# Performance work log

Hardware: AMD Instinct MI355X
Metric: run time of the kernel (lower is better)

## Reference

```python
import jax, jax.numpy as jnp
import numpy as np

B, T, D, U = 64, 512, 512, 512


def setup_inputs() -> dict:
    key = jax.random.key(0)
    ks = jax.random.split(key, 8)
    s_in = 1.0 / np.sqrt(D)
    s_rec = 1.0 / np.sqrt(U)
    return {
        "xf": jax.random.normal(ks[0], (B, T, D), jnp.float32),
        "xb": jax.random.normal(ks[1], (B, T, D), jnp.float32),
        "Wf": jax.random.normal(ks[2], (D, 4 * U), jnp.float32) * s_in,
        "Uf": jax.random.normal(ks[3], (U, 4 * U), jnp.float32) * s_rec,
        "bf": jnp.zeros((4 * U,), jnp.float32),
        "Wb": jax.random.normal(ks[4], (D, 4 * U), jnp.float32) * s_in,
        "Ub": jax.random.normal(ks[5], (U, 4 * U), jnp.float32) * s_rec,
        "bb": jnp.zeros((4 * U,), jnp.float32),
    }


def _lstm(x, W, Urec, b):
    # x: [B,T,D]; Keras gate order i,f,g,o. Inference mode: dropout inactive.
    u = Urec.shape[0]
    xz = jnp.einsum("btd,dk->btk", x, W) + b  # precompute input projection [B,T,4u]
    xz = jnp.swapaxes(xz, 0, 1)  # [T,B,4u] for scan

    def step(carry, z_t):
        h, c = carry
        z = z_t + h @ Urec  # [B,4u]
        i = jax.nn.sigmoid(z[:, :u])
        f = jax.nn.sigmoid(z[:, u:2 * u])
        g = jnp.tanh(z[:, 2 * u:3 * u])
        o = jax.nn.sigmoid(z[:, 3 * u:])
        c = f * c + i * g
        h = o * jnp.tanh(c)
        return (h, c), h

    nb = x.shape[0]
    h0 = jnp.zeros((nb, u), x.dtype)
    c0 = jnp.zeros((nb, u), x.dtype)
    _, hs = jax.lax.scan(step, (h0, c0), xz)  # hs: [T,B,u]
    return jnp.swapaxes(hs, 0, 1)  # [B,T,u]


def reference(xf, xb, Wf, Uf, bf, Wb, Ub, bb):
    fwd = _lstm(xf, Wf, Uf, bf)
    bwd = _lstm(xb, Wb, Ub, bb)
    return jnp.concatenate([fwd, bwd], axis=-1)  # [B,T,2U]
```

## Files before the change

kernel.cpp:

```cpp
#include <hip/hip_runtime.h>
#include <stdint.h>


typedef _Float16 f16;
typedef _Float16 f16x8 __attribute__((ext_vector_type(8)));
typedef float    f32x4 __attribute__((ext_vector_type(4)));
typedef unsigned long long u64;

typedef __attribute__((address_space(1))) const void* gas_ptr;
typedef __attribute__((address_space(3))) void* las_ptr;

__device__ inline void gl_lds16(const void* g, void* l) {
    __builtin_amdgcn_global_load_lds((gas_ptr)g, (las_ptr)l, 16, 0, 0);
}

#define SENT64 0x7F7F7F7F7F7F7F7FULL


__global__ void k_cvt(const float* __restrict__ src, f16* __restrict__ dst, int n8) {
    int i = blockIdx.x * 256 + threadIdx.x;
    if (i >= n8) return;
    const float4* s = (const float4*)src;
    float4 a = s[2 * i], b = s[2 * i + 1];
    f16x8 o = {(f16)a.x, (f16)a.y, (f16)a.z, (f16)a.w,
               (f16)b.x, (f16)b.y, (f16)b.z, (f16)b.w};
    *(f16x8*)(dst + 8 * (size_t)i) = o;
}

__global__ void k_tcvt(const float* __restrict__ src, f16* __restrict__ dst) {
    int tid = blockIdx.x * 256 + threadIdx.x;
    int kc = tid >> 11;
    int n  = tid & 2047;
    f16x8 o;
#pragma unroll
    for (int j = 0; j < 8; ++j)
        o[j] = (f16)src[(size_t)(kc * 8 + j) * 2048 + n];
    *(f16x8*)(dst + (size_t)n * 512 + kc * 8) = o;
}


__global__ void k_fill(f16* __restrict__ ring, int CT, int zero0) {
    size_t i = ((size_t)blockIdx.x * 256 + threadIdx.x) * 8;
    const size_t slot = 65536;
    size_t total = (size_t)(CT + 1) * slot;
    if (i >= total) return;
    u64 fillv = SENT64;
    if (i < slot) { if (!zero0) return; fillv = 0; }
    union { u64 u[2]; f16x8 v; } t; t.u[0] = fillv; t.u[1] = fillv;
    *(f16x8*)(ring + i) = t.v;
}

__global__ void k_copyslot(f16* __restrict__ ring, int CT) {
    size_t i = (size_t)(blockIdx.x * 256 + threadIdx.x) * 8;
    f16x8 v = *(const f16x8*)(ring + (size_t)CT * 65536 + i);
    *(f16x8*)(ring + i) = v;
}


__global__ __launch_bounds__(256) void k_proj(
    const f16* __restrict__ x16, const f16* __restrict__ WT,
    const float* __restrict__ bfw, const float* __restrict__ bbw,
    f16* __restrict__ xz, int t0, int CT, int lct) {
    __shared__ f16 smem[16384];
    f16* As = smem;
    f16* Bs = smem + 8192;

    const int tid = threadIdx.x;
    const int l = tid & 63, v = tid >> 6;
    const int mt = blockIdx.x, nt = blockIdx.y, d = blockIdx.z;
    const int wm = v >> 1, wn = v & 1;
    const int lr4 = l >> 4, c16 = l & 15;

    f32x4 acc[4][4];
#pragma unroll
    for (int i = 0; i < 4; ++i)
#pragma unroll
        for (int j = 0; j < 4; ++j) acc[i][j] = (f32x4)0.f;

    auto stage = [&](int kk, int buf) {
#pragma unroll
        for (int rd = 0; rd < 2; ++rd) {
            int idx = rd * 256 + tid;
            int r = idx >> 2, kp = idx & 3;
            int m = mt * 128 + r;
            int b = m >> lct, tc = m & (CT - 1);
            const f16* ga = x16 + (((size_t)(d * 64 + b) * 512 + (t0 + tc)) * 512 + kk * 32 + kp * 8);
            gl_lds16(ga, &As[buf * 4096 + (rd * 256 + v * 64) * 8]);
        }
#pragma unroll
        for (int rd = 0; rd < 2; ++rd) {
            int idx = rd * 256 + tid;
            int r = idx >> 2, kp = idx & 3;
            const f16* gb = WT + ((size_t)(d * 2048 + nt * 128 + r) * 512 + kk * 32 + kp * 8);
            gl_lds16(gb, &Bs[buf * 4096 + (rd * 256 + v * 64) * 8]);
        }
    };

    stage(0, 0);
    for (int kk = 0; kk < 16; ++kk) {
        __syncthreads();
        if (kk < 15) stage(kk + 1, (kk + 1) & 1);
        int buf = kk & 1;
        f16x8 af[4], bfr[4];
#pragma unroll
        for (int mf = 0; mf < 4; ++mf)
            af[mf] = *(const f16x8*)&As[buf * 4096 + (wm * 64 + mf * 16 + c16) * 32 + lr4 * 8];
#pragma unroll
        for (int nf = 0; nf < 4; ++nf)
            bfr[nf] = *(const f16x8*)&Bs[buf * 4096 + (wn * 64 + nf * 16 + c16) * 32 + lr4 * 8];
#pragma unroll
        for (int mf = 0; mf < 4; ++mf)
#pragma unroll
            for (int nf = 0; nf < 4; ++nf)
                acc[mf][nf] = __builtin_amdgcn_mfma_f32_16x16x32_f16(af[mf], bfr[nf], acc[mf][nf], 0, 0, 0);
    }
    __syncthreads();

    const float* bias = d ? bbw : bfw;
    float bv[4];
#pragma unroll
    for (int nf = 0; nf < 4; ++nf) bv[nf] = bias[nt * 128 + wn * 64 + nf * 16 + c16];

    f16* Cs = smem;
#pragma unroll
    for (int mf = 0; mf < 4; ++mf)
#pragma unroll
        for (int nf = 0; nf < 4; ++nf)
#pragma unroll
            for (int r = 0; r < 4; ++r) {
                int row = wm * 64 + mf * 16 + lr4 * 4 + r;
                int col = wn * 64 + nf * 16 + c16;
                Cs[row * 128 + col] = (f16)(acc[mf][nf][r] + bv[nf]);
            }
    __syncthreads();
#pragma unroll
    for (int ch = 0; ch < 8; ++ch) {
        int flat = ch * 256 + tid;
        int row = flat >> 4, cc = flat & 15;
        int m = mt * 128 + row;
        int b = m >> lct, tc = m & (CT - 1);
        f16x8 val = *(const f16x8*)&Cs[row * 128 + cc * 8];
        *(f16x8*)&xz[((size_t)(d * 64 + b) * CT + tc) * 2048 + nt * 128 + cc * 8] = val;
    }
}


__global__ __launch_bounds__(256, 1) void k_recur(
    const f16* __restrict__ xz, const f16* __restrict__ UT,
    f16* __restrict__ ring, float* __restrict__ cbuf,
    float* __restrict__ out, int t0, int CT) {
    __shared__ f16 xzsm[2][2048];
    __shared__ f16 wsm[4][128];
    __shared__ f16 hsm[8192];

    const int tid = threadIdx.x;
    const int l = tid & 63, v = tid >> 6;
    const int bx = blockIdx.x;
    const int d   = bx >> 6;
    const int grp = (bx >> 4) & 3;
    const int wg  = bx & 15;
    const int wu0 = wg * 32;
    const int lr4 = l >> 4;
    const int du  = (l & 15) >> 2;
    const int gid = l & 3;
    const int gidx = d * 4 + grp;

    int unitloc[2], nstd[2];
#pragma unroll
    for (int nf = 0; nf < 2; ++nf) {
        int u = wu0 + v * 8 + nf * 4 + du;
        unitloc[nf] = v * 8 + nf * 4 + du;
        nstd[nf] = gid * 512 + u;
    }

    f16x8 Ufr[2][16];
#pragma unroll
    for (int nf = 0; nf < 2; ++nf)
#pragma unroll
        for (int kk = 0; kk < 16; ++kk)
            Ufr[nf][kk] = *(const f16x8*)&UT[((size_t)d * 2048 + nstd[nf]) * 512 + kk * 32 + lr4 * 8];

    float cst[2][4];
#pragma unroll
    for (int nf = 0; nf < 2; ++nf)
#pragma unroll
        for (int r = 0; r < 4; ++r)
            cst[nf][r] = cbuf[((size_t)d * 64 + grp * 16 + lr4 * 4 + r) * 512 + (wu0 + v * 8 + nf * 4 + du)];

    {
        int row = tid >> 4, gate = (tid >> 2) & 3, u8 = tid & 3;
        const f16* g = xz + (((size_t)(d * 64 + grp * 16 + row) * CT + 0) * 2048 + gate * 512 + wu0 + u8 * 8);
        gl_lds16(g, &xzsm[0][v * 512]);
    }

    __syncthreads();

    for (int tl = 0; tl < CT; ++tl) {
        const int gt = t0 + tl;

        f32x4 acc0, acc1;
#pragma unroll
        for (int r = 0; r < 4; ++r) {
            acc0[r] = (float)xzsm[tl & 1][((lr4 * 4 + r) * 4 + gid) * 32 + unitloc[0]];
            acc1[r] = (float)xzsm[tl & 1][((lr4 * 4 + r) * 4 + gid) * 32 + unitloc[1]];
        }

        {
            int tnext = (tl + 1 < CT) ? tl + 1 : tl;
            int row = tid >> 4, gate = (tid >> 2) & 3, u8 = tid & 3;
            const f16* g = xz + (((size_t)(d * 64 + grp * 16 + row) * CT + tnext) * 2048 + gate * 512 + wu0 + u8 * 8);
            gl_lds16(g, &xzsm[tnext & 1][v * 512]);
        }

        const u64* sbase = (const u64*)ring + (size_t)tl * 16384 + (size_t)gidx * 2048
                         + (size_t)(v * 4) * 128 + l * 2;
        u64 g0, g1, g2, g3, g4, g5, g6, g7;
        while (true) {
            g0 = __hip_atomic_load(sbase +   0, __ATOMIC_RELAXED, __HIP_MEMORY_SCOPE_AGENT);
            g1 = __hip_atomic_load(sbase +   1, __ATOMIC_RELAXED, __HIP_MEMORY_SCOPE_AGENT);
            g2 = __hip_atomic_load(sbase + 128, __ATOMIC_RELAXED, __HIP_MEMORY_SCOPE_AGENT);
            g3 = __hip_atomic_load(sbase + 129, __ATOMIC_RELAXED, __HIP_MEMORY_SCOPE_AGENT);
            g4 = __hip_atomic_load(sbase + 256, __ATOMIC_RELAXED, __HIP_MEMORY_SCOPE_AGENT);
            g5 = __hip_atomic_load(sbase + 257, __ATOMIC_RELAXED, __HIP_MEMORY_SCOPE_AGENT);
            g6 = __hip_atomic_load(sbase + 384, __ATOMIC_RELAXED, __HIP_MEMORY_SCOPE_AGENT);
            g7 = __hip_atomic_load(sbase + 385, __ATOMIC_RELAXED, __HIP_MEMORY_SCOPE_AGENT);
            unsigned bad = (g0 == SENT64) | (g1 == SENT64) | (g2 == SENT64) | (g3 == SENT64)
                         | (g4 == SENT64) | (g5 == SENT64) | (g6 == SENT64) | (g7 == SENT64);
            if (!__any(bad)) break;
            __builtin_amdgcn_s_sleep(1);
        }

        {
            u64 gg[4][2] = {{g0, g1}, {g2, g3}, {g4, g5}, {g6, g7}};
#pragma unroll
            for (int jj = 0; jj < 4; ++jj) {
                union { u64 u[2]; f16x8 v8; } t; t.u[0] = gg[jj][0]; t.u[1] = gg[jj][1];
                int byte = (v * 4 + jj) * 1024 + l * 16;
                byte ^= ((l >> 2) & 7) << 4;
                *(f16x8*)((char*)hsm + byte) = t.v8;
            }
        }
        __syncthreads();

#pragma unroll
        for (int j = 0; j < 16; ++j) {
            int byte = j * 1024 + (l & 15) * 64 + lr4 * 16;
            byte ^= (l & 7) << 4;
            f16x8 a = *(const f16x8*)((const char*)hsm + byte);
            acc0 = __builtin_amdgcn_mfma_f32_16x16x32_f16(a, Ufr[0][j], acc0, 0, 0, 0);
            acc1 = __builtin_amdgcn_mfma_f32_16x16x32_f16(a, Ufr[1][j], acc1, 0, 0, 0);
        }

        float act[2][4];
#pragma unroll
        for (int nf = 0; nf < 2; ++nf)
#pragma unroll
            for (int r = 0; r < 4; ++r) {
                float z = nf ? acc1[r] : acc0[r];
                float zz = (gid == 2) ? 2.f * z : z;
                float r0 = 1.f / (1.f + __expf(-zz));
                act[nf][r] = (gid == 2) ? 2.f * r0 - 1.f : r0;
            }

#pragma unroll
        for (int nf = 0; nf < 2; ++nf)
#pragma unroll
            for (int r = 0; r < 4; ++r) {
                float a0 = act[nf][r];
                float a1 = __shfl_xor(a0, 1);
                float a2 = __shfl_xor(a0, 2);
                float a3 = __shfl_xor(a0, 3);
                int mi = gid, mf_ = gid ^ 1, mg = gid ^ 2, mo = gid ^ 3;
                float iv = mi == 0 ? a0 : mi == 1 ? a1 : mi == 2 ? a2 : a3;
                float fv = mf_ == 0 ? a0 : mf_ == 1 ? a1 : mf_ == 2 ? a2 : a3;
                float gv = mg == 0 ? a0 : mg == 1 ? a1 : mg == 2 ? a2 : a3;
                float ov = mo == 0 ? a0 : mo == 1 ? a1 : mo == 2 ? a2 : a3;
                float cn = fv * cst[nf][r] + iv * gv;
                cst[nf][r] = cn;
                if (gid == 0) {
                    float th = copysignf(1.f - 2.f / (__expf(2.f * fabsf(cn)) + 1.f), cn);
                    wsm[v][(nf * 4 + du) * 16 + lr4 * 4 + r] = (f16)(ov * th);
                }
            }

        if (l < 16) {
            f16x8 hv8;
#pragma unroll
            for (int j = 0; j < 8; ++j) hv8[j] = wsm[v][j * 16 + l];
            f16* dst = ring + (size_t)(tl + 1) * 65536 + (size_t)gidx * 8192
                     + ((size_t)wg * 16 + l) * 32 + v * 8;
            union { u64 u[2]; f16x8 v8; } t; t.v8 = hv8;
            __hip_atomic_store((u64*)dst + 0, t.u[0], __ATOMIC_RELAXED, __HIP_MEMORY_SCOPE_AGENT);
            __hip_atomic_store((u64*)dst + 1, t.u[1], __ATOMIC_RELAXED, __HIP_MEMORY_SCOPE_AGENT);
            size_t ob = ((size_t)(grp * 16 + l) * 512 + gt) * 1024 + d * 512 + wu0 + v * 8;
            float4 o0 = {(float)hv8[0], (float)hv8[1], (float)hv8[2], (float)hv8[3]};
            float4 o1 = {(float)hv8[4], (float)hv8[5], (float)hv8[6], (float)hv8[7]};
            *(float4*)&out[ob] = o0;
            *(float4*)&out[ob + 4] = o1;
        }

        __syncthreads();
    }

    if (gid == 0) {
#pragma unroll
        for (int nf = 0; nf < 2; ++nf)
#pragma unroll
            for (int r = 0; r < 4; ++r)
                cbuf[((size_t)d * 64 + grp * 16 + lr4 * 4 + r) * 512 + (wu0 + v * 8 + nf * 4 + du)] = cst[nf][r];
    }
}


extern "C" void kernel_launch(void* const* d_in, const int* in_sizes, int n_in,
                              void* d_out, int out_size, void* d_ws, size_t ws_size,
                              hipStream_t stream) {
    const float* xf = (const float*)d_in[0];
    const float* xb = (const float*)d_in[1];
    const float* Wf = (const float*)d_in[2];
    const float* Uf = (const float*)d_in[3];
    const float* bf = (const float*)d_in[4];
    const float* Wb = (const float*)d_in[5];
    const float* Ub = (const float*)d_in[6];
    const float* bb = (const float*)d_in[7];
    float* out = (float*)d_out;

    char* ws = (char*)d_ws;
    size_t off = 0;
    auto alloc = [&](size_t bytes) { size_t o = off; off = (off + bytes + 255) & ~(size_t)255; return o; };
    size_t o_x16 = alloc((size_t)2 * 64 * 512 * 512 * 2);
    size_t o_wt  = alloc((size_t)2 * 2048 * 512 * 2);
    size_t o_ut  = alloc((size_t)2 * 2048 * 512 * 2);
    size_t o_cb  = alloc((size_t)2 * 64 * 512 * 4);
    size_t fixed = off;
    int CT = 512;
    while (CT > 32 && fixed + (size_t)(CT + 1) * 131072 + (size_t)2 * 64 * CT * 2048 * 2 > ws_size) CT >>= 1;
    size_t o_ring = alloc((size_t)(CT + 1) * 131072);
    size_t o_xz   = alloc((size_t)2 * 64 * CT * 2048 * 2);
    int lct = (CT == 512) ? 9 : (CT == 256) ? 8 : (CT == 128) ? 7 : (CT == 64) ? 6 : 5;

    f16* x16 = (f16*)(ws + o_x16);
    f16* wt16 = (f16*)(ws + o_wt);
    f16* ut16 = (f16*)(ws + o_ut);
    float* cb = (float*)(ws + o_cb);
    f16* ring = (f16*)(ws + o_ring);
    f16* xzp  = (f16*)(ws + o_xz);

    const int n8 = 16777216 / 8;
    k_cvt<<<8192, 256, 0, stream>>>(xf, x16, n8);
    k_cvt<<<8192, 256, 0, stream>>>(xb, x16 + (size_t)16777216, n8);
    k_tcvt<<<512, 256, 0, stream>>>(Wf, wt16);
    k_tcvt<<<512, 256, 0, stream>>>(Wb, wt16 + (size_t)2048 * 512);
    k_tcvt<<<512, 256, 0, stream>>>(Uf, ut16);
    k_tcvt<<<512, 256, 0, stream>>>(Ub, ut16 + (size_t)2048 * 512);
    hipMemsetAsync(cb, 0, (size_t)2 * 64 * 512 * 4, stream);

    int nch = 512 / CT;
    int fillgrid = (int)(((size_t)(CT + 1) * 65536 / 8 + 255) / 256);
    for (int c = 0; c < nch; ++c) {
        int t0 = c * CT;
        k_proj<<<dim3(64 * CT / 128, 16, 2), 256, 0, stream>>>(x16, wt16, bf, bb, xzp, t0, CT, lct);
        if (c > 0) k_copyslot<<<32, 256, 0, stream>>>(ring, CT);
        k_fill<<<fillgrid, 256, 0, stream>>>(ring, CT, c == 0 ? 1 : 0);
        const f16* a_xz = xzp; const f16* a_ut = ut16;
        f16* a_ring = ring; float* a_cb = cb; float* a_out = out;
        int a_t0 = t0, a_ct = CT;
        void* args[7] = {&a_xz, &a_ut, &a_ring, &a_cb, &a_out, &a_t0, &a_ct};
        hipLaunchCooperativeKernel((void*)k_recur, dim3(128), dim3(256), args, 0u, stream);
    }
}
```

Baseline: 2.525 ms.

## Repartition LSTM recurrence to fewer larger workgroups with double-buffered h

The recurrent kernel moves from 128 blocks of 256 threads (32 units each) to 32 blocks of 512 threads (128 units each), with 4 gate-fragments per wave held in registers. The hidden-state LDS tile is double-buffered so the trailing per-step barrier is removed. The xz input-projection is read straight from global into registers instead of via an async LDS prefetch. Each wave now publishes its h slice with one 64-bit store per lane. The aim is fewer cross-block ring polls and less synchronisation per timestep. The cost is higher register pressure and fewer CUs doing the serial recurrence.

```diff
diff --git a/kernel.cpp b/kernel.cpp
--- a/kernel.cpp
+++ b/kernel.cpp
@@ -145,169 +145,154 @@
 }
 
 
-__global__ __launch_bounds__(256, 1) void k_recur(
+__global__ __launch_bounds__(512, 1) void k_recur(
     const f16* __restrict__ xz, const f16* __restrict__ UT,
     f16* __restrict__ ring, float* __restrict__ cbuf,
     float* __restrict__ out, int t0, int CT) {
-    __shared__ f16 xzsm[2][2048];
-    __shared__ f16 wsm[4][128];
-    __shared__ f16 hsm[8192];
+    __shared__ __align__(16) f16 hsm[2][8192];
+    __shared__ f16 wsm[8][256];
 
     const int tid = threadIdx.x;
-    const int l = tid & 63, v = tid >> 6;
+    const int l = tid & 63, w = tid >> 6;
     const int bx = blockIdx.x;
-    const int d   = bx >> 6;
-    const int grp = (bx >> 4) & 3;
-    const int wg  = bx & 15;
-    const int wu0 = wg * 32;
+    const int d   = bx >> 4;
+    const int grp = (bx >> 2) & 3;
+    const int p   = bx & 3;
+    const int gidx = d * 4 + grp;
+    const int row16 = l & 15;
     const int lr4 = l >> 4;
     const int du  = (l & 15) >> 2;
     const int gid = l & 3;
-    const int gidx = d * 4 + grp;
-
-    int unitloc[2], nstd[2];
-#pragma unroll
-    for (int nf = 0; nf < 2; ++nf) {
-        int u = wu0 + v * 8 + nf * 4 + du;
-        unitloc[nf] = v * 8 + nf * 4 + du;
-        nstd[nf] = gid * 512 + u;
-    }
-
-    f16x8 Ufr[2][16];
-#pragma unroll
-    for (int nf = 0; nf < 2; ++nf)
+    const int ub  = p * 128 + w * 16;
+    const int kb0 = 2 * w, kb1 = 2 * w + 1;
+    const int mykb = p * 4 + (w >> 1);
+    const int sw16 = (lr4 ^ ((row16 >> 1) & 3)) << 4;
+
+    f16x8 Ufr[4][16];
+#pragma unroll
+    for (int nf = 0; nf < 4; ++nf) {
+        int nstd = gid * 512 + ub + nf * 4 + du;
 #pragma unroll
         for (int kk = 0; kk < 16; ++kk)
-            Ufr[nf][kk] = *(const f16x8*)&UT[((size_t)d * 2048 + nstd[nf]) * 512 + kk * 32 + lr4 * 8];
-
-    float cst[2][4];
-#pragma unroll
-    for (int nf = 0; nf < 2; ++nf)
+            Ufr[nf][kk] = *(const f16x8*)&UT[((size_t)d * 2048 + nstd) * 512 + kk * 32 + lr4 * 8];
+    }
+
+    float cst[4][4];
+#pragma unroll
+    for (int nf = 0; nf < 4; ++nf)
 #pragma unroll
         for (int r = 0; r < 4; ++r)
-            cst[nf][r] = cbuf[((size_t)d * 64 + grp * 16 + lr4 * 4 + r) * 512 + (wu0 + v * 8 + nf * 4 + du)];
-
-    {
-        int row = tid >> 4, gate = (tid >> 2) & 3, u8 = tid & 3;
-        const f16* g = xz + (((size_t)(d * 64 + grp * 16 + row) * CT + 0) * 2048 + gate * 512 + wu0 + u8 * 8);
-        gl_lds16(g, &xzsm[0][v * 512]);
-    }
-
-    __syncthreads();
+            cst[nf][r] = cbuf[((size_t)d * 64 + grp * 16 + lr4 * 4 + r) * 512 + ub + nf * 4 + du];
 
     for (int tl = 0; tl < CT; ++tl) {
         const int gt = t0 + tl;
 
-        f32x4 acc0, acc1;
-#pragma unroll
-        for (int r = 0; r < 4; ++r) {
-            acc0[r] = (float)xzsm[tl & 1][((lr4 * 4 + r) * 4 + gid) * 32 + unitloc[0]];
-            acc1[r] = (float)xzsm[tl & 1][((lr4 * 4 + r) * 4 + gid) * 32 + unitloc[1]];
-        }
-
-        {
-            int tnext = (tl + 1 < CT) ? tl + 1 : tl;
-            int row = tid >> 4, gate = (tid >> 2) & 3, u8 = tid & 3;
-            const f16* g = xz + (((size_t)(d * 64 + grp * 16 + row) * CT + tnext) * 2048 + gate * 512 + wu0 + u8 * 8);
-            gl_lds16(g, &xzsm[tnext & 1][v * 512]);
-        }
-
-        const u64* sbase = (const u64*)ring + (size_t)tl * 16384 + (size_t)gidx * 2048
-                         + (size_t)(v * 4) * 128 + l * 2;
-        u64 g0, g1, g2, g3, g4, g5, g6, g7;
+        const u64* pb = (const u64*)ring + (size_t)tl * 16384 + (size_t)gidx * 2048;
+        const size_t o0 = (size_t)kb0 * 128 + row16 * 8 + lr4 * 2;
+        const size_t o1 = (size_t)kb1 * 128 + row16 * 8 + lr4 * 2;
+        u64 a0, a1, b0, b1;
         while (true) {
-            g0 = __hip_atomic_load(sbase +   0, __ATOMIC_RELAXED, __HIP_MEMORY_SCOPE_AGENT);
-            g1 = __hip_atomic_load(sbase +   1, __ATOMIC_RELAXED, __HIP_MEMORY_SCOPE_AGENT);
-            g2 = __hip_atomic_load(sbase + 128, __ATOMIC_RELAXED, __HIP_MEMORY_SCOPE_AGENT);
-            g3 = __hip_atomic_load(sbase + 129, __ATOMIC_RELAXED, __HIP_MEMORY_SCOPE_AGENT);
-            g4 = __hip_atomic_load(sbase + 256, __ATOMIC_RELAXED, __HIP_MEMORY_SCOPE_AGENT);
-            g5 = __hip_atomic_load(sbase + 257, __ATOMIC_RELAXED, __HIP_MEMORY_SCOPE_AGENT);
-            g6 = __hip_atomic_load(sbase + 384, __ATOMIC_RELAXED, __HIP_MEMORY_SCOPE_AGENT);
-            g7 = __hip_atomic_load(sbase + 385, __ATOMIC_RELAXED, __HIP_MEMORY_SCOPE_AGENT);
-            unsigned bad = (g0 == SENT64) | (g1 == SENT64) | (g2 == SENT64) | (g3 == SENT64)
-                         | (g4 == SENT64) | (g5 == SENT64) | (g6 == SENT64) | (g7 == SENT64);
+            a0 = __hip_atomic_load(pb + o0,     __ATOMIC_RELAXED, __HIP_MEMORY_SCOPE_AGENT);
+            a1 = __hip_atomic_load(pb + o0 + 1, __ATOMIC_RELAXED, __HIP_MEMORY_SCOPE_AGENT);
+            b0 = __hip_atomic_load(pb + o1,     __ATOMIC_RELAXED, __HIP_MEMORY_SCOPE_AGENT);
+            b1 = __hip_atomic_load(pb + o1 + 1, __ATOMIC_RELAXED, __HIP_MEMORY_SCOPE_AGENT);
+            unsigned bad = (a0 == SENT64) | (a1 == SENT64) | (b0 == SENT64) | (b1 == SENT64);
             if (!__any(bad)) break;
             __builtin_amdgcn_s_sleep(1);
         }
 
         {
-            u64 gg[4][2] = {{g0, g1}, {g2, g3}, {g4, g5}, {g6, g7}};
-#pragma unroll
-            for (int jj = 0; jj < 4; ++jj) {
-                union { u64 u[2]; f16x8 v8; } t; t.u[0] = gg[jj][0]; t.u[1] = gg[jj][1];
-                int byte = (v * 4 + jj) * 1024 + l * 16;
-                byte ^= ((l >> 2) & 7) << 4;
-                *(f16x8*)((char*)hsm + byte) = t.v8;
-            }
-        }
+            char* hw = (char*)&hsm[tl & 1][0];
+            union { u64 u[2]; f16x8 v; } ta, tb;
+            ta.u[0] = a0; ta.u[1] = a1;
+            tb.u[0] = b0; tb.u[1] = b1;
+            *(f16x8*)(hw + kb0 * 1024 + row16 * 64 + sw16) = ta.v;
+            *(f16x8*)(hw + kb1 * 1024 + row16 * 64 + sw16) = tb.v;
+        }
+
+        f16x8 xzr[4][2];
+#pragma unroll
+        for (int r = 0; r < 4; ++r)
+#pragma unroll
+            for (int m = 0; m < 2; ++m)
+                xzr[r][m] = *(const f16x8*)&xz[((size_t)(d * 64 + grp * 16 + lr4 * 4 + r) * CT + tl) * 2048
+                                               + gid * 512 + ub + m * 8];
+
         __syncthreads();
 
+        f32x4 acc[4];
+#pragma unroll
+        for (int nf = 0; nf < 4; ++nf) acc[nf] = (f32x4)0.f;
+        const char* hb = (const char*)&hsm[tl & 1][0];
 #pragma unroll
         for (int j = 0; j < 16; ++j) {
-            int byte = j * 1024 + (l & 15) * 64 + lr4 * 16;
-            byte ^= (l & 7) << 4;
-            f16x8 a = *(const f16x8*)((const char*)hsm + byte);
-            acc0 = __builtin_amdgcn_mfma_f32_16x16x32_f16(a, Ufr[0][j], acc0, 0, 0, 0);
-            acc1 = __builtin_amdgcn_mfma_f32_16x16x32_f16(a, Ufr[1][j], acc1, 0, 0, 0);
-        }
-
-        float act[2][4];
-#pragma unroll
-        for (int nf = 0; nf < 2; ++nf)
+            f16x8 a = *(const f16x8*)(hb + j * 1024 + row16 * 64 + sw16);
+#pragma unroll
+            for (int nf = 0; nf < 4; ++nf)
+                acc[nf] = __builtin_amdgcn_mfma_f32_16x16x32_f16(a, Ufr[nf][j], acc[nf], 0, 0, 0);
+        }
+
+        float act[4][4];
+#pragma unroll
+        for (int nf = 0; nf < 4; ++nf) {
 #pragma unroll
             for (int r = 0; r < 4; ++r) {
-                float z = nf ? acc1[r] : acc0[r];
+                union { f16x8 v; u64 u[2]; } xw; xw.v = xzr[r][nf >> 1];
+                u64 word = xw.u[nf & 1];
+                union { unsigned short s; f16 h; } cv;
+                cv.s = (unsigned short)(word >> (du * 16));
+                float z = acc[nf][r] + (float)cv.h;
                 float zz = (gid == 2) ? 2.f * z : z;
                 float r0 = 1.f / (1.f + __expf(-zz));
                 act[nf][r] = (gid == 2) ? 2.f * r0 - 1.f : r0;
             }
-
-#pragma unroll
-        for (int nf = 0; nf < 2; ++nf)
+        }
+
+#pragma unroll
+        for (int nf = 0; nf < 4; ++nf)
 #pragma unroll
             for (int r = 0; r < 4; ++r) {
-                float a0 = act[nf][r];
-                float a1 = __shfl_xor(a0, 1);
-                float a2 = __shfl_xor(a0, 2);
-                float a3 = __shfl_xor(a0, 3);
+                float a0f = act[nf][r];
+                float a1f = __shfl_xor(a0f, 1);
+                float a2f = __shfl_xor(a0f, 2);
+                float a3f = __shfl_xor(a0f, 3);
                 int mi = gid, mf_ = gid ^ 1, mg = gid ^ 2, mo = gid ^ 3;
-                float iv = mi == 0 ? a0 : mi == 1 ? a1 : mi == 2 ? a2 : a3;
-                float fv = mf_ == 0 ? a0 : mf_ == 1 ? a1 : mf_ == 2 ? a2 : a3;
-                float gv = mg == 0 ? a0 : mg == 1 ? a1 : mg == 2 ? a2 : a3;
-                float ov = mo == 0 ? a0 : mo == 1 ? a1 : mo == 2 ? a2 : a3;
+                float iv = mi == 0 ? a0f : mi == 1 ? a1f : mi == 2 ? a2f : a3f;
+                float fv = mf_ == 0 ? a0f : mf_ == 1 ? a1f : mf_ == 2 ? a2f : a3f;
+                float gv = mg == 0 ? a0f : mg == 1 ? a1f : mg == 2 ? a2f : a3f;
+                float ov = mo == 0 ? a0f : mo == 1 ? a1f : mo == 2 ? a2f : a3f;
                 float cn = fv * cst[nf][r] + iv * gv;
                 cst[nf][r] = cn;
                 if (gid == 0) {
                     float th = copysignf(1.f - 2.f / (__expf(2.f * fabsf(cn)) + 1.f), cn);
-                    wsm[v][(nf * 4 + du) * 16 + lr4 * 4 + r] = (f16)(ov * th);
+                    wsm[w][(nf * 4 + du) * 16 + lr4 * 4 + r] = (f16)(ov * th);
                 }
             }
 
-        if (l < 16) {
-            f16x8 hv8;
-#pragma unroll
-            for (int j = 0; j < 8; ++j) hv8[j] = wsm[v][j * 16 + l];
-            f16* dst = ring + (size_t)(tl + 1) * 65536 + (size_t)gidx * 8192
-                     + ((size_t)wg * 16 + l) * 32 + v * 8;
-            union { u64 u[2]; f16x8 v8; } t; t.v8 = hv8;
-            __hip_atomic_store((u64*)dst + 0, t.u[0], __ATOMIC_RELAXED, __HIP_MEMORY_SCOPE_AGENT);
-            __hip_atomic_store((u64*)dst + 1, t.u[1], __ATOMIC_RELAXED, __HIP_MEMORY_SCOPE_AGENT);
-            size_t ob = ((size_t)(grp * 16 + l) * 512 + gt) * 1024 + d * 512 + wu0 + v * 8;
-            float4 o0 = {(float)hv8[0], (float)hv8[1], (float)hv8[2], (float)hv8[3]};
-            float4 o1 = {(float)hv8[4], (float)hv8[5], (float)hv8[6], (float)hv8[7]};
-            *(float4*)&out[ob] = o0;
-            *(float4*)&out[ob + 4] = o1;
-        }
-
-        __syncthreads();
+        {
+            union { unsigned short s[4]; u64 u; } pk;
+            float hf[4];
+#pragma unroll
+            for (int k = 0; k < 4; ++k) {
+                union { f16 h; unsigned short s; } cv;
+                cv.h = wsm[w][(lr4 * 4 + k) * 16 + row16];
+                pk.s[k] = cv.s;
+                hf[k] = (float)cv.h;
+            }
+            u64* qdst = (u64*)ring + (size_t)(tl + 1) * 16384 + (size_t)gidx * 2048
+                      + (size_t)mykb * 128 + row16 * 8 + ((w & 1) * 4 + lr4);
+            __hip_atomic_store(qdst, pk.u, __ATOMIC_RELAXED, __HIP_MEMORY_SCOPE_AGENT);
+            float4 o4 = {hf[0], hf[1], hf[2], hf[3]};
+            *(float4*)&out[((size_t)(grp * 16 + row16) * 512 + gt) * 1024 + d * 512 + ub + lr4 * 4] = o4;
+        }
     }
 
     if (gid == 0) {
 #pragma unroll
-        for (int nf = 0; nf < 2; ++nf)
+        for (int nf = 0; nf < 4; ++nf)
 #pragma unroll
             for (int r = 0; r < 4; ++r)
-                cbuf[((size_t)d * 64 + grp * 16 + lr4 * 4 + r) * 512 + (wu0 + v * 8 + nf * 4 + du)] = cst[nf][r];
+                cbuf[((size_t)d * 64 + grp * 16 + lr4 * 4 + r) * 512 + ub + nf * 4 + du] = cst[nf][r];
     }
 }
 
@@ -366,6 +351,6 @@
         f16* a_ring = ring; float* a_cb = cb; float* a_out = out;
         int a_t0 = t0, a_ct = CT;
         void* args[7] = {&a_xz, &a_ut, &a_ring, &a_cb, &a_out, &a_t0, &a_ct};
-        hipLaunchCooperativeKernel((void*)k_recur, dim3(128), dim3(256), args, 0u, stream);
-    }
-}
+        hipLaunchCooperativeKernel((void*)k_recur, dim3(32), dim3(512), args, 0u, stream);
+    }
+}
```

Measured after the change: 7.390 ms. 2.93x slower.

## Double-buffer recurrent h tile in LDS and prefetch xz into registers

Applied to the files above, without the earlier changes.

The shared h tile becomes double-buffered by timestep parity, which lets the trailing per-step barrier be dropped so each step has one __syncthreads. The xz input projection is no longer staged through LDS with async global_load_lds; each lane loads its own slice into registers for the next step and adds it after the MFMA chain, with accumulators starting at zero. The U-weight preload is rewritten as relaxed atomic 64-bit loads. This aims to cut barrier and LDS traffic on the latency-bound recurrent critical path, at the cost of more LDS and register pressure. It relies on wsm reuse staying safe without the second barrier.

```diff
diff --git a/kernel.cpp b/kernel.cpp
--- a/kernel.cpp
+++ b/kernel.cpp
@@ -149,9 +149,8 @@
     const f16* __restrict__ xz, const f16* __restrict__ UT,
     f16* __restrict__ ring, float* __restrict__ cbuf,
     float* __restrict__ out, int t0, int CT) {
-    __shared__ f16 xzsm[2][2048];
+    __shared__ __align__(16) f16 hsm[2][8192];
     __shared__ f16 wsm[4][128];
-    __shared__ f16 hsm[8192];
 
     const int tid = threadIdx.x;
     const int l = tid & 63, v = tid >> 6;
@@ -164,21 +163,21 @@
     const int du  = (l & 15) >> 2;
     const int gid = l & 3;
     const int gidx = d * 4 + grp;
-
-    int unitloc[2], nstd[2];
+    const int row16 = l & 15;
+
+    f16x8 Ufr[2][16];
 #pragma unroll
     for (int nf = 0; nf < 2; ++nf) {
-        int u = wu0 + v * 8 + nf * 4 + du;
-        unitloc[nf] = v * 8 + nf * 4 + du;
-        nstd[nf] = gid * 512 + u;
-    }
-
-    f16x8 Ufr[2][16];
-#pragma unroll
-    for (int nf = 0; nf < 2; ++nf)
-#pragma unroll
-        for (int kk = 0; kk < 16; ++kk)
-            Ufr[nf][kk] = *(const f16x8*)&UT[((size_t)d * 2048 + nstd[nf]) * 512 + kk * 32 + lr4 * 8];
+        int nstd = gid * 512 + wu0 + v * 8 + nf * 4 + du;
+#pragma unroll
+        for (int kk = 0; kk < 16; ++kk) {
+            const u64* q = (const u64*)(UT + ((size_t)d * 2048 + nstd) * 512 + kk * 32 + lr4 * 8);
+            union { u64 u[2]; f16x8 v8; } t;
+            t.u[0] = __hip_atomic_load(q + 0, __ATOMIC_RELAXED, __HIP_MEMORY_SCOPE_WORKGROUP);
+            t.u[1] = __hip_atomic_load(q + 1, __ATOMIC_RELAXED, __HIP_MEMORY_SCOPE_WORKGROUP);
+            Ufr[nf][kk] = t.v8;
+        }
+    }
 
     float cst[2][4];
 #pragma unroll
@@ -187,30 +186,14 @@
         for (int r = 0; r < 4; ++r)
             cst[nf][r] = cbuf[((size_t)d * 64 + grp * 16 + lr4 * 4 + r) * 512 + (wu0 + v * 8 + nf * 4 + du)];
 
-    {
-        int row = tid >> 4, gate = (tid >> 2) & 3, u8 = tid & 3;
-        const f16* g = xz + (((size_t)(d * 64 + grp * 16 + row) * CT + 0) * 2048 + gate * 512 + wu0 + u8 * 8);
-        gl_lds16(g, &xzsm[0][v * 512]);
-    }
-
-    __syncthreads();
+    f16x8 xzr[4];
+#pragma unroll
+    for (int r = 0; r < 4; ++r)
+        xzr[r] = *(const f16x8*)&xz[((size_t)(d * 64 + grp * 16 + lr4 * 4 + r) * CT + 0) * 2048
+                                    + gid * 512 + wu0 + v * 8];
 
     for (int tl = 0; tl < CT; ++tl) {
         const int gt = t0 + tl;
-
-        f32x4 acc0, acc1;
-#pragma unroll
-        for (int r = 0; r < 4; ++r) {
-            acc0[r] = (float)xzsm[tl & 1][((lr4 * 4 + r) * 4 + gid) * 32 + unitloc[0]];
-            acc1[r] = (float)xzsm[tl & 1][((lr4 * 4 + r) * 4 + gid) * 32 + unitloc[1]];
-        }
-
-        {
-            int tnext = (tl + 1 < CT) ? tl + 1 : tl;
-            int row = tid >> 4, gate = (tid >> 2) & 3, u8 = tid & 3;
-            const f16* g = xz + (((size_t)(d * 64 + grp * 16 + row) * CT + tnext) * 2048 + gate * 512 + wu0 + u8 * 8);
-            gl_lds16(g, &xzsm[tnext & 1][v * 512]);
-        }
 
         const u64* sbase = (const u64*)ring + (size_t)tl * 16384 + (size_t)gidx * 2048
                          + (size_t)(v * 4) * 128 + l * 2;
@@ -231,22 +214,26 @@
         }
 
         {
+            char* hw = (char*)&hsm[tl & 1][0];
             u64 gg[4][2] = {{g0, g1}, {g2, g3}, {g4, g5}, {g6, g7}};
 #pragma unroll
             for (int jj = 0; jj < 4; ++jj) {
                 union { u64 u[2]; f16x8 v8; } t; t.u[0] = gg[jj][0]; t.u[1] = gg[jj][1];
                 int byte = (v * 4 + jj) * 1024 + l * 16;
                 byte ^= ((l >> 2) & 7) << 4;
-                *(f16x8*)((char*)hsm + byte) = t.v8;
+                *(f16x8*)(hw + byte) = t.v8;
             }
         }
+
         __syncthreads();
 
+        f32x4 acc0 = (f32x4)0.f, acc1 = (f32x4)0.f;
+        const char* hb = (const char*)&hsm[tl & 1][0];
 #pragma unroll
         for (int j = 0; j < 16; ++j) {
-            int byte = j * 1024 + (l & 15) * 64 + lr4 * 16;
+            int byte = j * 1024 + row16 * 64 + lr4 * 16;
             byte ^= (l & 7) << 4;
-            f16x8 a = *(const f16x8*)((const char*)hsm + byte);
+            f16x8 a = *(const f16x8*)(hb + byte);
             acc0 = __builtin_amdgcn_mfma_f32_16x16x32_f16(a, Ufr[0][j], acc0, 0, 0, 0);
             acc1 = __builtin_amdgcn_mfma_f32_16x16x32_f16(a, Ufr[1][j], acc1, 0, 0, 0);
         }
@@ -256,7 +243,10 @@
         for (int nf = 0; nf < 2; ++nf)
 #pragma unroll
             for (int r = 0; r < 4; ++r) {
-                float z = nf ? acc1[r] : acc0[r];
+                union { f16x8 v8; u64 u[2]; } xw; xw.v8 = xzr[r];
+                union { unsigned short s; f16 h; } cv;
+                cv.s = (unsigned short)(xw.u[nf] >> (du * 16));
+                float z = (nf ? acc1[r] : acc0[r]) + (float)cv.h;
                 float zz = (gid == 2) ? 2.f * z : z;
                 float r0 = 1.f / (1.f + __expf(-zz));
                 act[nf][r] = (gid == 2) ? 2.f * r0 - 1.f : r0;
@@ -266,15 +256,15 @@
         for (int nf = 0; nf < 2; ++nf)
 #pragma unroll
             for (int r = 0; r < 4; ++r) {
-                float a0 = act[nf][r];
-                float a1 = __shfl_xor(a0, 1);
-                float a2 = __shfl_xor(a0, 2);
-                float a3 = __shfl_xor(a0, 3);
+                float a0f = act[nf][r];
+                float a1f = __shfl_xor(a0f, 1);
+                float a2f = __shfl_xor(a0f, 2);
+                float a3f = __shfl_xor(a0f, 3);
                 int mi = gid, mf_ = gid ^ 1, mg = gid ^ 2, mo = gid ^ 3;
-                float iv = mi == 0 ? a0 : mi == 1 ? a1 : mi == 2 ? a2 : a3;
-                float fv = mf_ == 0 ? a0 : mf_ == 1 ? a1 : mf_ == 2 ? a2 : a3;
-                float gv = mg == 0 ? a0 : mg == 1 ? a1 : mg == 2 ? a2 : a3;
-                float ov = mo == 0 ? a0 : mo == 1 ? a1 : mo == 2 ? a2 : a3;
+                float iv = mi == 0 ? a0f : mi == 1 ? a1f : mi == 2 ? a2f : a3f;
+                float fv = mf_ == 0 ? a0f : mf_ == 1 ? a1f : mf_ == 2 ? a2f : a3f;
+                float gv = mg == 0 ? a0f : mg == 1 ? a1f : mg == 2 ? a2f : a3f;
+                float ov = mo == 0 ? a0f : mo == 1 ? a1f : mo == 2 ? a2f : a3f;
                 float cn = fv * cst[nf][r] + iv * gv;
                 cst[nf][r] = cn;
                 if (gid == 0) {
@@ -299,7 +289,13 @@
             *(float4*)&out[ob + 4] = o1;
         }
 
-        __syncthreads();
+        {
+            int tn = (tl + 1 < CT) ? tl + 1 : tl;
+#pragma unroll
+            for (int r = 0; r < 4; ++r)
+                xzr[r] = *(const f16x8*)&xz[((size_t)(d * 64 + grp * 16 + lr4 * 4 + r) * CT + tn) * 2048
+                                            + gid * 512 + wu0 + v * 8];
+        }
     }
 
     if (gid == 0) {
```

Result: slower. 2.792 ms (+10.6%).
